# Performance work log

Hardware: AMD Instinct MI355X
Metric: run time of the kernel (lower is better)

Reference implementation:

```python
import jax, jax.numpy as jnp
import numpy as np


def setup_inputs() -> dict:
    key = jax.random.key(0)
    k1, k2 = jax.random.split(key)
    B, N, M, C = 32, 4096, 4096, 3
    xyz1 = jax.random.normal(k1, (B, N, C), dtype=jnp.float32)
    xyz2 = jax.random.normal(k2, (B, M, C), dtype=jnp.float32)
    return {"xyz1": xyz1, "xyz2": xyz2}


def _chamfer_l2(xyz1, xyz2):
    # Pairwise squared L2 distances via ||a||^2 + ||b||^2 - 2 a.b  (b n m)
    sq1 = jnp.sum(xyz1 * xyz1, axis=-1)            # [B, N]
    sq2 = jnp.sum(xyz2 * xyz2, axis=-1)            # [B, M]
    cross = jnp.einsum('bnc,bmc->bnm', xyz1, xyz2) # [B, N, M]
    d = sq1[:, :, None] + sq2[:, None, :] - 2.0 * cross
    dist1 = jnp.min(d, axis=2)                     # [B, N] nearest in xyz2
    dist2 = jnp.min(d, axis=1)                     # [B, M] nearest in xyz1
    return jnp.mean(dist1, axis=-1) + jnp.mean(dist2, axis=-1)  # [B]


def reference(xyz1, xyz2):
    return _chamfer_l2(xyz1, xyz2)
```

## Files before the change

### kernel.cpp

```cpp
#include <hip/hip_runtime.h>

typedef _Float16 half8 __attribute__((ext_vector_type(8)));
typedef float floatx16 __attribute__((ext_vector_type(16)));

#define TPB   256
#define RPTS  1024
#define NTILE (RPTS / 32)
#define SMH   (RPTS * 16)

__global__ __launch_bounds__(TPB, 4) void chamfer_mfma(const float* __restrict__ xyz1,
                                                       const float* __restrict__ xyz2,
                                                       float* __restrict__ out,
                                                       int N, int M) {
    const int b = blockIdx.y, dir = blockIdx.z;
    const float* __restrict__ P = dir ? xyz2 + (size_t)b * M * 3 : xyz1 + (size_t)b * N * 3;
    const float* __restrict__ Q = dir ? xyz1 + (size_t)b * N * 3 : xyz2 + (size_t)b * M * 3;
    const int nq = dir ? M : N;
    const int md = dir ? N : M;

    if ((int)blockIdx.x * TPB >= nq) return;

    __shared__ __align__(16) _Float16 smB[SMH];

    const int tid = (int)threadIdx.x;
    const int w   = tid >> 6;
    const int l   = tid & 63;
    const int m   = l & 31;
    const int h   = l >> 5;

    const _Float16 hz = (_Float16)0.0f, hone = (_Float16)1.0f;
    const int qb = blockIdx.x * 256 + w * 64;

    half8 afr[2];
#pragma unroll
    for (int g = 0; g < 2; ++g) {
        int idx = qb + g * 32 + m;
        int ci  = idx < nq ? idx : nq - 1;
        float x = P[3 * ci], y = P[3 * ci + 1], z = P[3 * ci + 2];
        _Float16 xh = (_Float16)x, yh = (_Float16)y, zh = (_Float16)z;
        _Float16 xl = (_Float16)(x - (float)xh);
        _Float16 yl = (_Float16)(y - (float)yh);
        _Float16 zl = (_Float16)(z - (float)zh);
        half8 a;
        if (h == 0) {
            a[0] = -xh; a[1] = -xh; a[2] = -xl; a[3] = -yh;
            a[4] = -yh; a[5] = -yl; a[6] = -zh; a[7] = -zh;
        } else {
            a[0] = -zl; a[1] = hone; a[2] = hone; a[3] = hz;
            a[4] = hz;  a[5] = hz;   a[6] = hz;  a[7] = hz;
        }
        afr[g] = a;
    }

    float rm[32];
#pragma unroll
    for (int i = 0; i < 32; ++i) rm[i] = 3.0e38f;

    const floatx16 czero = {0.0f, 0.0f, 0.0f, 0.0f, 0.0f, 0.0f, 0.0f, 0.0f,
                            0.0f, 0.0f, 0.0f, 0.0f, 0.0f, 0.0f, 0.0f, 0.0f};
    const int nrounds = (md + RPTS - 1) / RPTS;
    const _Float16* bp = smB + h * 256 + m * 8;

    for (int r = 0; r < nrounds; ++r) {
        if (r) __syncthreads();
#pragma unroll
        for (int k = 0; k < RPTS / TPB; ++k) {
            int j = tid + k * TPB;
            int g = r * RPTS + j;
            g = g < md ? g : md - 1;
            float x = Q[3 * g], y = Q[3 * g + 1], z = Q[3 * g + 2];
            float hq = 0.5f * (x * x + y * y + z * z);
            _Float16 xh = (_Float16)x, yh = (_Float16)y, zh = (_Float16)z;
            _Float16 xl = (_Float16)(x - (float)xh);
            _Float16 yl = (_Float16)(y - (float)yh);
            _Float16 zl = (_Float16)(z - (float)zh);
            _Float16 qh = (_Float16)hq;
            _Float16 ql = (_Float16)(hq - (float)qh);
            int t = j >> 5, c = j & 31;
            half8 v0, v1;
            v0[0] = xh; v0[1] = xl; v0[2] = xh; v0[3] = yh;
            v0[4] = yl; v0[5] = yh; v0[6] = zh; v0[7] = zl;
            v1[0] = zh; v1[1] = qh; v1[2] = ql; v1[3] = hz;
            v1[4] = hz; v1[5] = hz; v1[6] = hz; v1[7] = hz;
            *(half8*)&smB[t * 512 + c * 8]       = v0;
            *(half8*)&smB[t * 512 + 256 + c * 8] = v1;
        }
        __syncthreads();

        for (int t = 0; t < NTILE; t += 2) {
            half8 b0 = *(const half8*)(bp + t * 512);
            half8 b1 = *(const half8*)(bp + t * 512 + 512);
            floatx16 d0a = __builtin_amdgcn_mfma_f32_32x32x16_f16(afr[0], b0, czero, 0, 0, 0);
            floatx16 d0b = __builtin_amdgcn_mfma_f32_32x32x16_f16(afr[0], b1, czero, 0, 0, 0);
#pragma unroll
            for (int i = 0; i < 16; ++i)
                rm[i] = fminf(fminf(rm[i], d0a[i]), d0b[i]);
            floatx16 d1a = __builtin_amdgcn_mfma_f32_32x32x16_f16(afr[1], b0, czero, 0, 0, 0);
            floatx16 d1b = __builtin_amdgcn_mfma_f32_32x32x16_f16(afr[1], b1, czero, 0, 0, 0);
#pragma unroll
            for (int i = 0; i < 16; ++i)
                rm[16 + i] = fminf(fminf(rm[16 + i], d1a[i]), d1b[i]);
        }
    }

#pragma unroll
    for (int off = 1; off < 32; off <<= 1) {
#pragma unroll
        for (int i = 0; i < 32; ++i) rm[i] = fminf(rm[i], __shfl_xor(rm[i], off, 64));
    }

    float s = 0.0f;
    if (m < 16) {
        const int reg = (m & 3) + 4 * (m >> 2);
        const int row = 4 * h + (m & 3) + 8 * (m >> 2);
#pragma unroll
        for (int g = 0; g < 2; ++g) {
            int idx = qb + g * 32 + row;
            if (idx < nq) {
                float x = P[3 * idx], y = P[3 * idx + 1], z = P[3 * idx + 2];
                s += rm[g * 16 + reg] + 0.5f * (x * x + y * y + z * z);
            }
        }
    }
#pragma unroll
    for (int off = 32; off > 0; off >>= 1) s += __shfl_down(s, off, 64);
    if (l == 0) atomicAdd(out + b, s * (2.0f / (float)nq));
}

extern "C" void kernel_launch(void* const* d_in, const int* in_sizes, int n_in,
                              void* d_out, int out_size, void* d_ws, size_t ws_size,
                              hipStream_t stream) {
    const float* xyz1 = (const float*)d_in[0];
    const float* xyz2 = (const float*)d_in[1];
    float* out = (float*)d_out;

    const int B = out_size;
    const int N = in_sizes[0] / (3 * B);
    const int M = in_sizes[1] / (3 * B);

    hipMemsetAsync(d_out, 0, (size_t)B * sizeof(float), stream);

    const int qmax = N > M ? N : M;
    dim3 grid((qmax + 255) / 256, B, 2);
    chamfer_mfma<<<grid, dim3(TPB), 0, stream>>>(xyz1, xyz2, out, N, M);
}
```

Baseline: 116.4 us.

## Halve queries per wave and block to cut registers and raise occupancy

Each wave now processes one 32-query MFMA A-fragment instead of two, so the running-minimum array shrinks from 32 to 16 floats. Blocks cover 128 queries, the grid doubles, and the staged reference chunk shrinks to 512 points. Launch bounds rise to 8 blocks per CU to allow more resident waves to hide latency. The trade-off is that each B fragment read from LDS now feeds half as many MFMAs, and every reference point is converted and staged twice as often across the grid.

```diff
diff --git a/kernel.cpp b/kernel.cpp
--- a/kernel.cpp
+++ b/kernel.cpp
@@ -4,11 +4,11 @@
 typedef float floatx16 __attribute__((ext_vector_type(16)));
 
 #define TPB   256
-#define RPTS  1024
+#define RPTS  512
 #define NTILE (RPTS / 32)
 #define SMH   (RPTS * 16)
 
-__global__ __launch_bounds__(TPB, 4) void chamfer_mfma(const float* __restrict__ xyz1,
+__global__ __launch_bounds__(TPB, 8) void chamfer_mfma(const float* __restrict__ xyz1,
                                                        const float* __restrict__ xyz2,
                                                        float* __restrict__ out,
                                                        int N, int M) {
@@ -18,7 +18,7 @@
     const int nq = dir ? M : N;
     const int md = dir ? N : M;
 
-    if ((int)blockIdx.x * TPB >= nq) return;
+    if ((int)blockIdx.x * 128 >= nq) return;
 
     __shared__ __align__(16) _Float16 smB[SMH];
 
@@ -29,32 +29,29 @@
     const int h   = l >> 5;
 
     const _Float16 hz = (_Float16)0.0f, hone = (_Float16)1.0f;
-    const int qb = blockIdx.x * 256 + w * 64;
+    const int qb = blockIdx.x * 128 + w * 32;
 
-    half8 afr[2];
-#pragma unroll
-    for (int g = 0; g < 2; ++g) {
-        int idx = qb + g * 32 + m;
+    half8 afr;
+    {
+        int idx = qb + m;
         int ci  = idx < nq ? idx : nq - 1;
         float x = P[3 * ci], y = P[3 * ci + 1], z = P[3 * ci + 2];
         _Float16 xh = (_Float16)x, yh = (_Float16)y, zh = (_Float16)z;
         _Float16 xl = (_Float16)(x - (float)xh);
         _Float16 yl = (_Float16)(y - (float)yh);
         _Float16 zl = (_Float16)(z - (float)zh);
-        half8 a;
         if (h == 0) {
-            a[0] = -xh; a[1] = -xh; a[2] = -xl; a[3] = -yh;
-            a[4] = -yh; a[5] = -yl; a[6] = -zh; a[7] = -zh;
+            afr[0] = -xh; afr[1] = -xh; afr[2] = -xl; afr[3] = -yh;
+            afr[4] = -yh; afr[5] = -yl; afr[6] = -zh; afr[7] = -zh;
         } else {
-            a[0] = -zl; a[1] = hone; a[2] = hone; a[3] = hz;
-            a[4] = hz;  a[5] = hz;   a[6] = hz;  a[7] = hz;
+            afr[0] = -zl; afr[1] = hone; afr[2] = hone; afr[3] = hz;
+            afr[4] = hz;  afr[5] = hz;   afr[6] = hz;  afr[7] = hz;
         }
-        afr[g] = a;
     }
 
-    float rm[32];
+    float rm[16];
 #pragma unroll
-    for (int i = 0; i < 32; ++i) rm[i] = 3.0e38f;
+    for (int i = 0; i < 16; ++i) rm[i] = 3.0e38f;
 
     const floatx16 czero = {0.0f, 0.0f, 0.0f, 0.0f, 0.0f, 0.0f, 0.0f, 0.0f,
                             0.0f, 0.0f, 0.0f, 0.0f, 0.0f, 0.0f, 0.0f, 0.0f};
@@ -90,36 +87,30 @@
         for (int t = 0; t < NTILE; t += 2) {
             half8 b0 = *(const half8*)(bp + t * 512);
             half8 b1 = *(const half8*)(bp + t * 512 + 512);
-            floatx16 d0a = __builtin_amdgcn_mfma_f32_32x32x16_f16(afr[0], b0, czero, 0, 0, 0);
-            floatx16 d0b = __builtin_amdgcn_mfma_f32_32x32x16_f16(afr[0], b1, czero, 0, 0, 0);
+            floatx16 da = __builtin_amdgcn_mfma_f32_32x32x16_f16(afr, b0, czero, 0, 0, 0);
+            floatx16 db = __builtin_amdgcn_mfma_f32_32x32x16_f16(afr, b1, czero, 0, 0, 0);
 #pragma unroll
             for (int i = 0; i < 16; ++i)
-                rm[i] = fminf(fminf(rm[i], d0a[i]), d0b[i]);
-            floatx16 d1a = __builtin_amdgcn_mfma_f32_32x32x16_f16(afr[1], b0, czero, 0, 0, 0);
-            floatx16 d1b = __builtin_amdgcn_mfma_f32_32x32x16_f16(afr[1], b1, czero, 0, 0, 0);
-#pragma unroll
-            for (int i = 0; i < 16; ++i)
-                rm[16 + i] = fminf(fminf(rm[16 + i], d1a[i]), d1b[i]);
+                rm[i] = fminf(fminf(rm[i], da[i]), db[i]);
         }
     }
 
 #pragma unroll
     for (int off = 1; off < 32; off <<= 1) {
 #pragma unroll
-        for (int i = 0; i < 32; ++i) rm[i] = fminf(rm[i], __shfl_xor(rm[i], off, 64));
+        for (int i = 0; i < 16; ++i) rm[i] = fminf(rm[i], __shfl_xor(rm[i], off, 64));
     }
 
     float s = 0.0f;
     if (m < 16) {
-        const int reg = (m & 3) + 4 * (m >> 2);
-        const int row = 4 * h + (m & 3) + 8 * (m >> 2);
+        const int row = (m & 3) + 8 * (m >> 2) + 4 * h;
+        const int idx = qb + row;
+        if (idx < nq) {
+            float v = rm[0];
 #pragma unroll
-        for (int g = 0; g < 2; ++g) {
-            int idx = qb + g * 32 + row;
-            if (idx < nq) {
-                float x = P[3 * idx], y = P[3 * idx + 1], z = P[3 * idx + 2];
-                s += rm[g * 16 + reg] + 0.5f * (x * x + y * y + z * z);
-            }
+            for (int r2 = 1; r2 < 16; ++r2) v = (m == r2) ? rm[r2] : v;
+            float x = P[3 * idx], y = P[3 * idx + 1], z = P[3 * idx + 2];
+            s = v + 0.5f * (x * x + y * y + z * z);
         }
     }
 #pragma unroll
@@ -141,6 +132,6 @@
     hipMemsetAsync(d_out, 0, (size_t)B * sizeof(float), stream);
 
     const int qmax = N > M ? N : M;
-    dim3 grid((qmax + 255) / 256, B, 2);
+    dim3 grid((qmax + 127) / 128, B, 2);
     chamfer_mfma<<<grid, dim3(TPB), 0, stream>>>(xyz1, xyz2, out, N, M);
 }
```

New measurement: 153.6 us. 1.32x slower.

## Prepack fp16 fragments in workspace and split reference range across blocks

Applied to the files above, without the earlier changes.

Adds a pre-pass that converts every point set once into the split-fp16 MFMA fragment layout in workspace, so the main kernel copies the packed tiles into LDS with plain vector loads instead of re-converting them in every block. The reference range is split across two blocks per query tile to double the grid. Partial minima are merged with atomicMin on order-preserving integer encodings, and a separate kernel then sums them. This costs extra launches, a memset and global traffic for the packed buffers and the distance array. The old path is kept as a fallback when the workspace is too small.

```diff
diff --git a/kernel.cpp b/kernel.cpp
--- a/kernel.cpp
+++ b/kernel.cpp
@@ -8,17 +8,60 @@
 #define NTILE (RPTS / 32)
 #define SMH   (RPTS * 16)
 
-__global__ __launch_bounds__(TPB, 4) void chamfer_mfma(const float* __restrict__ xyz1,
-                                                       const float* __restrict__ xyz2,
-                                                       float* __restrict__ out,
-                                                       int N, int M) {
+__device__ __forceinline__ unsigned enc(float f) {
+    int b = __float_as_int(f);
+    return (b >= 0) ? ((unsigned)b | 0x80000000u) : ~(unsigned)b;
+}
+__device__ __forceinline__ float dec(unsigned k) {
+    int b = (k & 0x80000000u) ? (int)(k & 0x7FFFFFFFu) : (int)~k;
+    return __int_as_float(b);
+}
+
+__global__ __launch_bounds__(256) void pack_frags(const float* __restrict__ src,
+                                                  _Float16* __restrict__ dst,
+                                                  int npts, int npad) {
+    const int b = blockIdx.y;
+    const int p = blockIdx.x * 256 + (int)threadIdx.x;
+    if (p >= npad) return;
+    const int g = p < npts ? p : npts - 1;
+    const float* sp = src + ((size_t)b * npts + g) * 3;
+    float x = sp[0], y = sp[1], z = sp[2];
+    float hq = 0.5f * (x * x + y * y + z * z);
+    _Float16 xh = (_Float16)x, yh = (_Float16)y, zh = (_Float16)z;
+    _Float16 xl = (_Float16)(x - (float)xh);
+    _Float16 yl = (_Float16)(y - (float)yh);
+    _Float16 zl = (_Float16)(z - (float)zh);
+    _Float16 qh = (_Float16)hq;
+    _Float16 ql = (_Float16)(hq - (float)qh);
+    const _Float16 hz = (_Float16)0.0f;
+    half8 v0, v1;
+    v0[0] = xh; v0[1] = xl; v0[2] = xh; v0[3] = yh;
+    v0[4] = yl; v0[5] = yh; v0[6] = zh; v0[7] = zl;
+    v1[0] = zh; v1[1] = qh; v1[2] = ql; v1[3] = hz;
+    v1[4] = hz; v1[5] = hz; v1[6] = hz; v1[7] = hz;
+    int t = p >> 5, c = p & 31;
+    _Float16* base = dst + (size_t)b * npad * 16 + (size_t)t * 512 + c * 8;
+    *(half8*)base         = v0;
+    *(half8*)(base + 256) = v1;
+}
+
+__global__ __launch_bounds__(TPB, 4) void chamfer_ws(const float* __restrict__ xyz1,
+                                                     const float* __restrict__ xyz2,
+                                                     const _Float16* __restrict__ frag1,
+                                                     const _Float16* __restrict__ frag2,
+                                                     unsigned* __restrict__ dist,
+                                                     int N, int M, int B,
+                                                     int p1pad, int p2pad, int qpad) {
     const int b = blockIdx.y, dir = blockIdx.z;
-    const float* __restrict__ P = dir ? xyz2 + (size_t)b * M * 3 : xyz1 + (size_t)b * N * 3;
-    const float* __restrict__ Q = dir ? xyz1 + (size_t)b * N * 3 : xyz2 + (size_t)b * M * 3;
-    const int nq = dir ? M : N;
-    const int md = dir ? N : M;
-
-    if ((int)blockIdx.x * TPB >= nq) return;
+    const float*    __restrict__ P = dir ? xyz2 + (size_t)b * M * 3 : xyz1 + (size_t)b * N * 3;
+    const _Float16* __restrict__ F = dir ? frag1 + (size_t)b * p1pad * 16
+                                         : frag2 + (size_t)b * p2pad * 16;
+    const int nq    = dir ? M : N;
+    const int mdpad = dir ? p1pad : p2pad;
+
+    const int qblk = blockIdx.x >> 1;
+    const int s    = blockIdx.x & 1;
+    if (qblk * 256 >= nq) return;
 
     __shared__ __align__(16) _Float16 smB[SMH];
 
@@ -29,7 +72,7 @@
     const int h   = l >> 5;
 
     const _Float16 hz = (_Float16)0.0f, hone = (_Float16)1.0f;
-    const int qb = blockIdx.x * 256 + w * 64;
+    const int qb = qblk * 256 + w * 64;
 
     half8 afr[2];
 #pragma unroll
@@ -58,9 +101,112 @@
 
     const floatx16 czero = {0.0f, 0.0f, 0.0f, 0.0f, 0.0f, 0.0f, 0.0f, 0.0f,
                             0.0f, 0.0f, 0.0f, 0.0f, 0.0f, 0.0f, 0.0f, 0.0f};
+    const int nrounds = mdpad / RPTS;
+    const _Float16* bp = smB + h * 256 + m * 8;
+
+    for (int r = s; r < nrounds; r += 2) {
+        if (r != s) __syncthreads();
+        const int4* __restrict__ gsrc = (const int4*)(F + (size_t)r * SMH);
+        int4* __restrict__ ldst = (int4*)smB;
+#pragma unroll
+        for (int k = 0; k < (SMH * 2 / 16) / TPB; ++k) {
+            int c = k * TPB + tid;
+            ldst[c] = gsrc[c];
+        }
+        __syncthreads();
+
+        for (int t = 0; t < NTILE; t += 2) {
+            half8 b0 = *(const half8*)(bp + t * 512);
+            half8 b1 = *(const half8*)(bp + t * 512 + 512);
+            floatx16 d0a = __builtin_amdgcn_mfma_f32_32x32x16_f16(afr[0], b0, czero, 0, 0, 0);
+            floatx16 d0b = __builtin_amdgcn_mfma_f32_32x32x16_f16(afr[0], b1, czero, 0, 0, 0);
+#pragma unroll
+            for (int i = 0; i < 16; ++i)
+                rm[i] = fminf(fminf(rm[i], d0a[i]), d0b[i]);
+            floatx16 d1a = __builtin_amdgcn_mfma_f32_32x32x16_f16(afr[1], b0, czero, 0, 0, 0);
+            floatx16 d1b = __builtin_amdgcn_mfma_f32_32x32x16_f16(afr[1], b1, czero, 0, 0, 0);
+#pragma unroll
+            for (int i = 0; i < 16; ++i)
+                rm[16 + i] = fminf(fminf(rm[16 + i], d1a[i]), d1b[i]);
+        }
+    }
+
+#pragma unroll
+    for (int off = 1; off < 32; off <<= 1) {
+#pragma unroll
+        for (int i = 0; i < 32; ++i) rm[i] = fminf(rm[i], __shfl_xor(rm[i], off, 64));
+    }
+
+    unsigned* dptr = dist + (size_t)(dir * B + b) * qpad;
+    if (m < 16) {
+        const int reg = (m & 3) + 4 * (m >> 2);
+        const int row = 4 * h + (m & 3) + 8 * (m >> 2);
+#pragma unroll
+        for (int g = 0; g < 2; ++g) {
+            int idx = qb + g * 32 + row;
+            if (idx < nq) {
+                float x = P[3 * idx], y = P[3 * idx + 1], z = P[3 * idx + 2];
+                float v = rm[g * 16 + reg] + 0.5f * (x * x + y * y + z * z);
+                atomicMin(dptr + idx, enc(v));
+            }
+        }
+    }
+}
+
+__global__ __launch_bounds__(256) void reduce_out(const unsigned* __restrict__ dist,
+                                                  float* __restrict__ out,
+                                                  int N, int M, int B, int qpad) {
+    const int b = blockIdx.x;
+    const int tid = (int)threadIdx.x;
+    float s = 0.0f;
+    const unsigned* d0 = dist + (size_t)b * qpad;
+    const unsigned* d1 = dist + (size_t)(B + b) * qpad;
+    for (int i = tid; i < N; i += 256) s += dec(d0[i]) * (1.0f / (float)N);
+    for (int i = tid; i < M; i += 256) s += dec(d1[i]) * (1.0f / (float)M);
+#pragma unroll
+    for (int off = 32; off > 0; off >>= 1) s += __shfl_down(s, off, 64);
+    __shared__ float red[4];
+    if ((tid & 63) == 0) red[tid >> 6] = s;
+    __syncthreads();
+    if (tid == 0) out[b] = 2.0f * (red[0] + red[1] + red[2] + red[3]);
+}
+
+__global__ __launch_bounds__(TPB, 4) void chamfer_plain(const float* __restrict__ xyz1,
+                                                        const float* __restrict__ xyz2,
+                                                        float* __restrict__ out,
+                                                        int N, int M) {
+    const int b = blockIdx.y, dir = blockIdx.z;
+    const float* __restrict__ P = dir ? xyz2 + (size_t)b * M * 3 : xyz1 + (size_t)b * N * 3;
+    const float* __restrict__ Q = dir ? xyz1 + (size_t)b * N * 3 : xyz2 + (size_t)b * M * 3;
+    const int nq = dir ? M : N;
+    const int md = dir ? N : M;
+    if ((int)blockIdx.x * TPB >= nq) return;
+    __shared__ __align__(16) _Float16 smB[SMH];
+    const int tid = (int)threadIdx.x;
+    const int w = tid >> 6, l = tid & 63, m = l & 31, h = l >> 5;
+    const _Float16 hz = (_Float16)0.0f, hone = (_Float16)1.0f;
+    const int qb = blockIdx.x * 256 + w * 64;
+    half8 afr[2];
+#pragma unroll
+    for (int g = 0; g < 2; ++g) {
+        int idx = qb + g * 32 + m;
+        int ci  = idx < nq ? idx : nq - 1;
+        float x = P[3 * ci], y = P[3 * ci + 1], z = P[3 * ci + 2];
+        _Float16 xh = (_Float16)x, yh = (_Float16)y, zh = (_Float16)z;
+        _Float16 xl = (_Float16)(x - (float)xh);
+        _Float16 yl = (_Float16)(y - (float)yh);
+        _Float16 zl = (_Float16)(z - (float)zh);
+        half8 a;
+        if (h == 0) { a[0]=-xh;a[1]=-xh;a[2]=-xl;a[3]=-yh;a[4]=-yh;a[5]=-yl;a[6]=-zh;a[7]=-zh; }
+        else        { a[0]=-zl;a[1]=hone;a[2]=hone;a[3]=hz;a[4]=hz;a[5]=hz;a[6]=hz;a[7]=hz; }
+        afr[g] = a;
+    }
+    float rm[32];
+#pragma unroll
+    for (int i = 0; i < 32; ++i) rm[i] = 3.0e38f;
+    const floatx16 czero = {0,0,0,0,0,0,0,0,0,0,0,0,0,0,0,0};
     const int nrounds = (md + RPTS - 1) / RPTS;
     const _Float16* bp = smB + h * 256 + m * 8;
-
     for (int r = 0; r < nrounds; ++r) {
         if (r) __syncthreads();
 #pragma unroll
@@ -78,37 +224,30 @@
             _Float16 ql = (_Float16)(hq - (float)qh);
             int t = j >> 5, c = j & 31;
             half8 v0, v1;
-            v0[0] = xh; v0[1] = xl; v0[2] = xh; v0[3] = yh;
-            v0[4] = yl; v0[5] = yh; v0[6] = zh; v0[7] = zl;
-            v1[0] = zh; v1[1] = qh; v1[2] = ql; v1[3] = hz;
-            v1[4] = hz; v1[5] = hz; v1[6] = hz; v1[7] = hz;
+            v0[0]=xh;v0[1]=xl;v0[2]=xh;v0[3]=yh;v0[4]=yl;v0[5]=yh;v0[6]=zh;v0[7]=zl;
+            v1[0]=zh;v1[1]=qh;v1[2]=ql;v1[3]=hz;v1[4]=hz;v1[5]=hz;v1[6]=hz;v1[7]=hz;
             *(half8*)&smB[t * 512 + c * 8]       = v0;
             *(half8*)&smB[t * 512 + 256 + c * 8] = v1;
         }
         __syncthreads();
-
         for (int t = 0; t < NTILE; t += 2) {
             half8 b0 = *(const half8*)(bp + t * 512);
             half8 b1 = *(const half8*)(bp + t * 512 + 512);
             floatx16 d0a = __builtin_amdgcn_mfma_f32_32x32x16_f16(afr[0], b0, czero, 0, 0, 0);
             floatx16 d0b = __builtin_amdgcn_mfma_f32_32x32x16_f16(afr[0], b1, czero, 0, 0, 0);
 #pragma unroll
-            for (int i = 0; i < 16; ++i)
-                rm[i] = fminf(fminf(rm[i], d0a[i]), d0b[i]);
+            for (int i = 0; i < 16; ++i) rm[i] = fminf(fminf(rm[i], d0a[i]), d0b[i]);
             floatx16 d1a = __builtin_amdgcn_mfma_f32_32x32x16_f16(afr[1], b0, czero, 0, 0, 0);
             floatx16 d1b = __builtin_amdgcn_mfma_f32_32x32x16_f16(afr[1], b1, czero, 0, 0, 0);
 #pragma unroll
-            for (int i = 0; i < 16; ++i)
-                rm[16 + i] = fminf(fminf(rm[16 + i], d1a[i]), d1b[i]);
-        }
-    }
-
+            for (int i = 0; i < 16; ++i) rm[16+i] = fminf(fminf(rm[16+i], d1a[i]), d1b[i]);
+        }
+    }
 #pragma unroll
     for (int off = 1; off < 32; off <<= 1) {
 #pragma unroll
         for (int i = 0; i < 32; ++i) rm[i] = fminf(rm[i], __shfl_xor(rm[i], off, 64));
     }
-
     float s = 0.0f;
     if (m < 16) {
         const int reg = (m & 3) + 4 * (m >> 2);
@@ -137,10 +276,31 @@
     const int B = out_size;
     const int N = in_sizes[0] / (3 * B);
     const int M = in_sizes[1] / (3 * B);
-
-    hipMemsetAsync(d_out, 0, (size_t)B * sizeof(float), stream);
-
     const int qmax = N > M ? N : M;
-    dim3 grid((qmax + 255) / 256, B, 2);
-    chamfer_mfma<<<grid, dim3(TPB), 0, stream>>>(xyz1, xyz2, out, N, M);
-}
+
+    const int p1pad = ((N + RPTS - 1) / RPTS) * RPTS;
+    const int p2pad = ((M + RPTS - 1) / RPTS) * RPTS;
+    const int qpad  = p1pad > p2pad ? p1pad : p2pad;
+    const size_t f1bytes = (size_t)B * p1pad * 32;
+    const size_t f2bytes = (size_t)B * p2pad * 32;
+    const size_t dbytes  = (size_t)2 * B * qpad * sizeof(unsigned);
+
+    if (ws_size >= f1bytes + f2bytes + dbytes) {
+        _Float16* frag1 = (_Float16*)d_ws;
+        _Float16* frag2 = (_Float16*)((char*)d_ws + f1bytes);
+        unsigned* dist  = (unsigned*)((char*)d_ws + f1bytes + f2bytes);
+
+        pack_frags<<<dim3(p1pad / 256, B), dim3(256), 0, stream>>>(xyz1, frag1, N, p1pad);
+        pack_frags<<<dim3(p2pad / 256, B), dim3(256), 0, stream>>>(xyz2, frag2, M, p2pad);
+        hipMemsetAsync(dist, 0xFF, dbytes, stream);
+
+        dim3 grid(((qmax + 255) / 256) * 2, B, 2);
+        chamfer_ws<<<grid, dim3(TPB), 0, stream>>>(xyz1, xyz2, frag1, frag2, dist,
+                                                   N, M, B, p1pad, p2pad, qpad);
+        reduce_out<<<dim3(B), dim3(256), 0, stream>>>(dist, out, N, M, B, qpad);
+    } else {
+        hipMemsetAsync(out, 0, (size_t)B * sizeof(float), stream);
+        dim3 grid((qmax + 255) / 256, B, 2);
+        chamfer_plain<<<grid, dim3(TPB), 0, stream>>>(xyz1, xyz2, out, N, M);
+    }
+}
```

Result: no change. 117.9 us (+1.3%).
